# Kernel optimization log

Hardware: AMD Instinct MI355X
Metric: run time of the kernel (lower is better)

## Reference

```python
import jax, jax.numpy as jnp
import numpy as np

N, IN_DIM, HEADS, OUT_DIM = 100000, 128, 4, 32
E = 1600000
NEG_SLOPE = 0.2

def setup_inputs() -> dict:
    key = jax.random.key(0)
    k1, k2, k3, k4, k5 = jax.random.split(key, 5)
    x = jax.random.normal(k1, (N, IN_DIM), dtype=jnp.float32)
    edge_index = jax.random.randint(k2, (2, E), 0, N, dtype=jnp.int32)
    # xavier-like init for params
    W = jax.random.uniform(k3, (IN_DIM, HEADS * OUT_DIM), dtype=jnp.float32,
                           minval=-1.0, maxval=1.0) * np.sqrt(6.0 / (IN_DIM + HEADS * OUT_DIM))
    a_src = jax.random.uniform(k4, (HEADS, OUT_DIM), dtype=jnp.float32,
                               minval=-1.0, maxval=1.0) * np.sqrt(6.0 / (HEADS + OUT_DIM))
    a_dst = jax.random.uniform(k5, (HEADS, OUT_DIM), dtype=jnp.float32,
                               minval=-1.0, maxval=1.0) * np.sqrt(6.0 / (HEADS + OUT_DIM))
    return {"x": x, "edge_index": edge_index, "W": W, "a_src": a_src, "a_dst": a_dst}

def reference(x, edge_index, W, a_src, a_dst):
    src, dst = edge_index[0], edge_index[1]
    n = x.shape[0]
    h = (x @ W).reshape(n, HEADS, OUT_DIM)                      # (N,H,D)
    # per-node attention score halves, then gather per edge (avoids E x D gather twice)
    s_src = jnp.einsum('nhd,hd->nh', h, a_src)                  # (N,H)
    s_dst = jnp.einsum('nhd,hd->nh', h, a_dst)                  # (N,H)
    e = s_src[src] + s_dst[dst]                                 # (E,H)
    e = jnp.where(e > 0, e, NEG_SLOPE * e)                      # leaky_relu(0.2)
    # segment softmax over edges sharing the same dst, per head
    max_per_dst = jax.ops.segment_max(e, dst, num_segments=n)   # (N,H)
    exp = jnp.exp(e - max_per_dst[dst])                         # (E,H)
    denom = jax.ops.segment_sum(exp, dst, num_segments=n)       # (N,H)
    alpha = exp / (denom[dst] + 1e-9)                           # (E,H)
    msg = h[src] * alpha[:, :, None]                            # (E,H,D)
    out = jax.ops.segment_sum(msg, dst, num_segments=n)         # (N,H,D)
    return out.reshape(n, HEADS * OUT_DIM)                      # concat=True
```

## Files before the change

kernel.cpp:

```cpp
#include <hip/hip_runtime.h>
#include <hip/hip_bf16.h>
#include <stdint.h>

#define N_NODES 100000
#define NE 1600000
#define NEG_SLOPE 0.2f
#define NSTRIP 6250
#define NGROUP 49
#define GCAP 34816
#define NFB 64
#define NBKT 3136
#define CAP 768
#define NCTR (NGROUP * 32 + NBKT)

typedef __attribute__((ext_vector_type(8))) short bf16x8;
typedef __attribute__((ext_vector_type(4))) float f32x4;
typedef __attribute__((ext_vector_type(2))) float f32x2;
typedef __attribute__((ext_vector_type(4))) uint32_t u32x4;
typedef __attribute__((ext_vector_type(2))) uint32_t u32x2;

__device__ __forceinline__ short f2bf(float f) {
    __hip_bfloat16 b = __float2bfloat16(f);
    short s; __builtin_memcpy(&s, &b, 2); return s;
}

__global__ __launch_bounds__(256) void k_prep(const float* __restrict__ W,
                                              const float* __restrict__ a_src,
                                              const float* __restrict__ a_dst,
                                              float* __restrict__ vv,
                                              short* __restrict__ wbf,
                                              int* __restrict__ ctrs) {
    const int t = threadIdx.x;
    if (blockIdx.x == 0) {
        if (t < 128) {
            const float* wrow = W + t * 128;
            #pragma unroll
            for (int hd = 0; hd < 4; ++hd) {
                float va = 0.f, vd = 0.f;
                #pragma unroll
                for (int d = 0; d < 32; ++d) {
                    float w = wrow[hd * 32 + d];
                    va += w * a_src[hd * 32 + d];
                    vd += w * a_dst[hd * 32 + d];
                }
                vv[t * 8 + hd]     = va;
                vv[t * 8 + 4 + hd] = vd;
            }
        }
        #pragma unroll 4
        for (int i = 0; i < 64; ++i) {
            int idx = t + i * 256;
            int k = idx >> 7, c = idx & 127;
            int byte = ((c << 8) + (k << 1)) ^ ((c & 7) << 4);
            *(short*)((char*)wbf + byte) = f2bf(W[idx]);
        }
    } else {
        for (int i = t; i < NCTR; i += 256) ctrs[i] = 0;
    }
}

__global__ __launch_bounds__(256) void k_gemm(const float* __restrict__ x,
                                              const short* __restrict__ wbf,
                                              const float* __restrict__ vv,
                                              unsigned char* __restrict__ h8,
                                              float* __restrict__ scales,
                                              float* __restrict__ sv) {
    __shared__ short wt[16384];
    __shared__ float vvl[1024];
    __shared__ float sc[64];
    const int t = threadIdx.x;

    {
        const int4* wsrc = (const int4*)wbf;
        int4* wdst = (int4*)wt;
        #pragma unroll
        for (int i = 0; i < 8; ++i) wdst[t + i * 256] = wsrc[t + i * 256];
    }
    *(f32x4*)(vvl + t * 4) = *(const f32x4*)(vv + t * 4);
    __syncthreads();

    const int wid = t >> 6, lane = t & 63;
    const int strip = blockIdx.x * 4 + wid;
    const bool active = strip < NSTRIP;
    const int r0 = strip * 16;
    const int lr = lane & 15, lg = lane >> 4;

    f32x4 acc[8];
    #pragma unroll
    for (int ct = 0; ct < 8; ++ct) acc[ct] = (f32x4){0.f, 0.f, 0.f, 0.f};
    float part[8];
    #pragma unroll
    for (int i = 0; i < 8; ++i) part[i] = 0.f;

    if (active) {
        bf16x8 a[4];
        #pragma unroll
        for (int kk = 0; kk < 4; ++kk) {
            const float* xp = x + (size_t)(r0 + lr) * 128 + kk * 32 + lg * 8;
            f32x4 x0 = *(const f32x4*)xp;
            f32x4 x1 = *(const f32x4*)(xp + 4);
            int kbase = kk * 32 + lg * 8;
            #pragma unroll
            for (int j = 0; j < 4; ++j) {
                a[kk][j]     = f2bf(x0[j]);
                a[kk][4 + j] = f2bf(x1[j]);
                f32x4 v0 = *(const f32x4*)(vvl + (kbase + j) * 8);
                f32x4 v1 = *(const f32x4*)(vvl + (kbase + j) * 8 + 4);
                f32x4 w0 = *(const f32x4*)(vvl + (kbase + 4 + j) * 8);
                f32x4 w1 = *(const f32x4*)(vvl + (kbase + 4 + j) * 8 + 4);
                #pragma unroll
                for (int i = 0; i < 4; ++i) {
                    part[i]     += x0[j] * v0[i] + x1[j] * w0[i];
                    part[4 + i] += x0[j] * v1[i] + x1[j] * w1[i];
                }
            }
        }
        #pragma unroll
        for (int ct = 0; ct < 8; ++ct) {
            int c = ct * 16 + lr;
            #pragma unroll
            for (int kk = 0; kk < 4; ++kk) {
                int byte = ((c << 8) + ((kk * 32 + lg * 8) << 1)) ^ ((c & 7) << 4);
                bf16x8 b = *(const bf16x8*)((char*)wt + byte);
                acc[ct] = __builtin_amdgcn_mfma_f32_16x16x32_bf16(a[kk], b, acc[ct], 0, 0, 0);
            }
        }
    }
    #pragma unroll
    for (int i = 0; i < 8; ++i) {
        part[i] += __shfl_xor(part[i], 16);
        part[i] += __shfl_xor(part[i], 32);
    }
    if (active && lg == 0) {
        f32x4 s0, s1;
        #pragma unroll
        for (int j = 0; j < 4; ++j) { s0[j] = part[j]; s1[j] = part[4 + j]; }
        *(f32x4*)(sv + (size_t)(r0 + lr) * 8)     = s0;
        *(f32x4*)(sv + (size_t)(r0 + lr) * 8 + 4) = s1;
    }
    if (active) {
        #pragma unroll
        for (int j = 0; j < 4; ++j) {
            float rm = 0.f;
            #pragma unroll
            for (int ct = 0; ct < 8; ++ct) rm = fmaxf(rm, fabsf(acc[ct][j]));
            #pragma unroll
            for (int off2 = 1; off2 < 16; off2 <<= 1)
                rm = fmaxf(rm, __shfl_xor(rm, off2));
            if (lr == 0) {
                scales[r0 + lg * 4 + j] = rm * (1.f / 127.f);
                sc[wid * 16 + lg * 4 + j] = 127.f / fmaxf(rm, 1e-20f);
            }
        }
    }
    __syncthreads();
    if (active) {
        #pragma unroll
        for (int ct = 0; ct < 8; ++ct) {
            #pragma unroll
            for (int j = 0; j < 4; ++j) {
                int row = wid * 16 + lg * 4 + j;
                wt[row * 128 + ct * 16 + lr] = f2bf(acc[ct][j]);
            }
        }
    }
    __syncthreads();
    const int R0 = blockIdx.x * 64;
    #pragma unroll
    for (int it = 0; it < 2; ++it) {
        int sidx = (it * 256 + t) * 16;
        int lrow = sidx >> 7, ch0 = sidx & 127;
        int grow = R0 + lrow;
        if (grow < N_NODES) {
            float invs = sc[lrow];
            u32x4 dws;
            #pragma unroll
            for (int d = 0; d < 4; ++d) {
                uint32_t dw = 0;
                #pragma unroll
                for (int bb = 0; bb < 4; ++bb) {
                    union { uint32_t i; float f; } uu;
                    uu.i = ((uint32_t)(uint16_t)wt[sidx + d * 4 + bb]) << 16;
                    float q = rintf(uu.f * invs);
                    q = fminf(fmaxf(q, -127.f), 127.f);
                    dw |= ((uint32_t)(int)(q + 128.f)) << (8 * bb);
                }
                dws[d] = dw;
            }
            *(u32x4*)(h8 + (size_t)grow * 128 + ch0) = dws;
        }
    }
}

__global__ __launch_bounds__(256) void k_part1(const int* __restrict__ ei,
                                               int* __restrict__ gcur,
                                               int* __restrict__ arena) {
    __shared__ int hist[NGROUP];
    __shared__ int lstart[NGROUP + 1];
    __shared__ int gb[NGROUP];
    __shared__ int binned[4096];
    const int t = threadIdx.x;
    const int e4b = blockIdx.x * 1024;
    if (t < NGROUP) hist[t] = 0;
    __syncthreads();
    int pk[16], gr[16], pl[16];
    #pragma unroll
    for (int i = 0; i < 4; ++i) {
        int e4 = e4b + i * 256 + t;
        bool v = e4 < NE / 4;
        int4 s4 = {0, 0, 0, 0}, d4 = {0, 0, 0, 0};
        if (v) {
            s4 = *(const int4*)(ei + (size_t)e4 * 4);
            d4 = *(const int4*)(ei + NE + (size_t)e4 * 4);
        }
#define P1(k, sf, df) { \
        if (v) { int g = (df) >> 11; gr[i*4+k] = g; \
                 pk[i*4+k] = ((sf) << 11) | ((df) & 2047); \
                 pl[i*4+k] = atomicAdd(&hist[g], 1); } else gr[i*4+k] = -1; }
        P1(0, s4.x, d4.x) P1(1, s4.y, d4.y) P1(2, s4.z, d4.z) P1(3, s4.w, d4.w)
#undef P1
    }
    __syncthreads();
    if (t < 64) {
        int v = (t < NGROUP) ? hist[t] : 0;
        int incl = v;
        #pragma unroll
        for (int off = 1; off < 64; off <<= 1) {
            int y = __shfl_up(incl, off);
            if (t >= off) incl += y;
        }
        if (t < NGROUP) lstart[t + 1] = incl;
        if (t == 0) lstart[0] = 0;
    }
    __syncthreads();
    if (t < NGROUP) gb[t] = atomicAdd(&gcur[t * 32], hist[t]);
    #pragma unroll
    for (int j = 0; j < 16; ++j)
        if (gr[j] >= 0) binned[lstart[gr[j]] + pl[j]] = pk[j];
    __syncthreads();
    const int lane = t & 63, wid = t >> 6;
    for (int g = wid; g < NGROUP; g += 4) {
        int base = gb[g];
        int n = min(hist[g], GCAP - base);
        const int ls = lstart[g];
        int* dst = arena + (size_t)g * GCAP + base;
        for (int i = lane; i < n; i += 64) dst[i] = binned[ls + i];
    }
}

__global__ __launch_bounds__(256) void k_part2(const int* __restrict__ gcur,
                                               const int* __restrict__ arena,
                                               int* __restrict__ bcur,
                                               int* __restrict__ tmp2) {
    const int g = blockIdx.x / 9, chunk = blockIdx.x - g * 9;
    const int cnt = min(gcur[g * 32], GCAP);
    const int cb = chunk * 4096;
    if (cb >= cnt) return;
    __shared__ int hist[NFB];
    __shared__ int lstart[NFB + 1];
    __shared__ int gb[NFB];
    __shared__ int binned[4096];
    const int t = threadIdx.x;
    if (t < NFB) hist[t] = 0;
    __syncthreads();
    int pk[16], fb[16], pl[16];
    const int* ga = arena + (size_t)g * GCAP;
    #pragma unroll
    for (int i = 0; i < 4; ++i) {
        int i4 = cb / 4 + i * 256 + t;
        bool v4 = (i4 * 4) < cnt;
        int4 w4 = {0, 0, 0, 0};
        if (v4) w4 = *(const int4*)(ga + (size_t)i4 * 4);
#define P2(k, wf) { int idx = i4 * 4 + k; \
        if (v4 && idx < cnt) { int f = ((wf) & 2047) >> 5; fb[i*4+k] = f; \
            pk[i*4+k] = (((wf) >> 11) << 5) | ((wf) & 31); \
            pl[i*4+k] = atomicAdd(&hist[f], 1); } else fb[i*4+k] = -1; }
        P2(0, w4.x) P2(1, w4.y) P2(2, w4.z) P2(3, w4.w)
#undef P2
    }
    __syncthreads();
    if (t < 64) {
        int v = hist[t];
        int incl = v;
        #pragma unroll
        for (int off = 1; off < 64; off <<= 1) {
            int y = __shfl_up(incl, off);
            if (t >= off) incl += y;
        }
        lstart[t + 1] = incl;
        if (t == 0) lstart[0] = 0;
    }
    __syncthreads();
    if (t < NFB) gb[t] = atomicAdd(&bcur[g * 64 + t], hist[t]);
    #pragma unroll
    for (int j = 0; j < 16; ++j)
        if (fb[j] >= 0) binned[lstart[fb[j]] + pl[j]] = pk[j];
    __syncthreads();
    const int lane = t & 63, wid = t >> 6;
    for (int f = wid; f < NFB; f += 4) {
        int base = gb[f];
        int n = min(hist[f], CAP - base);
        const int ls = lstart[f];
        int* dst = tmp2 + (size_t)(g * 64 + f) * CAP + base;
        for (int i = lane; i < n; i += 64) dst[i] = binned[ls + i];
    }
}

__global__ __launch_bounds__(256) void k_aggregate(const unsigned char* __restrict__ h8,
                                                   const float* __restrict__ scales,
                                                   const float* __restrict__ sv,
                                                   const int* __restrict__ bcur,
                                                   const int* __restrict__ tmp2,
                                                   float* __restrict__ out) {
    const int b = blockIdx.x;
    const int base = (b >> 6) * 2048 + (b & 63) * 32;
    if (base >= N_NODES) return;
    __shared__ int sorted[CAP];
    __shared__ float wbuf[CAP * 4];
    __shared__ float sbuf[CAP];
    __shared__ int cstart[33];
    __shared__ int ccnt[32];
    __shared__ f32x4 svd4[32];
    const int t = threadIdx.x;
    if (t < 32) {
        ccnt[t] = 0;
        svd4[t] = *(const f32x4*)(sv + (size_t)(base + t) * 8 + 4);
    }
    __syncthreads();
    const int cnt = min(bcur[b], CAP);
    const int* mytmp = tmp2 + (size_t)b * CAP;
    int e0 = -1, e1 = -1, e2 = -1, q0 = 0, q1 = 0, q2 = 0;
    if (t < cnt)       { e0 = mytmp[t];       q0 = atomicAdd(&ccnt[e0 & 31], 1); }
    if (t + 256 < cnt) { e1 = mytmp[t + 256]; q1 = atomicAdd(&ccnt[e1 & 31], 1); }
    if (t + 512 < cnt) { e2 = mytmp[t + 512]; q2 = atomicAdd(&ccnt[e2 & 31], 1); }
    __syncthreads();
    if (t < 64) {
        int v = (t < 32) ? ccnt[t] : 0;
        int incl = v;
        #pragma unroll
        for (int off = 1; off < 32; off <<= 1) {
            int y = __shfl_up(incl, off);
            if (t >= off) incl += y;
        }
        if (t < 32) cstart[t + 1] = incl;
        if (t == 0) cstart[0] = 0;
    }
    __syncthreads();
#define PLACE(e, q) { \
        int pos = cstart[(e) & 31] + (q); \
        sorted[pos] = (e); \
        sbuf[pos] = scales[(size_t)((e) >> 5)]; \
        f32x4 ss = *(const f32x4*)(sv + (size_t)((e) >> 5) * 8); \
        f32x4 sd = svd4[(e) & 31]; \
        f32x4 w4; \
        _Pragma("unroll") \
        for (int hh2 = 0; hh2 < 4; ++hh2) { \
            float v = ss[hh2] + sd[hh2]; \
            v = v > 0.f ? v : NEG_SLOPE * v; \
            w4[hh2] = __expf(v); \
        } \
        *(f32x4*)(wbuf + pos * 4) = w4; }
    if (e0 >= 0) PLACE(e0, q0)
    if (e1 >= 0) PLACE(e1, q1)
    if (e2 >= 0) PLACE(e2, q2)
#undef PLACE
    __syncthreads();

    const int lane = t & 63, wid = t >> 6;
    const int sg = lane >> 4, sl = lane & 15;
    const int hh = sl >> 2;
    const int sgid = wid * 4 + sg;
    const u32x2* hp2 = (const u32x2*)h8;
    #pragma unroll
    for (int rr = 0; rr < 2; ++rr) {
        const int r = sgid * 2 + rr;
        const int s0 = cstart[r], s1 = cstart[r + 1];
        f32x2 a01 = {0.f, 0.f}, a23 = {0.f, 0.f};
        f32x2 a45 = {0.f, 0.f}, a67 = {0.f, 0.f};
        float wsum = 0.f, aws = 0.f;
        for (int j = s0; j < s1; j += 4) {
            int j1 = j + 1 < s1 ? j + 1 : j;
            int j2 = j + 2 < s1 ? j + 2 : j;
            int j3 = j + 3 < s1 ? j + 3 : j;
            int eA = sorted[j], eB = sorted[j1], eC = sorted[j2], eD = sorted[j3];
            u32x2 p0 = hp2[(size_t)(eA >> 5) * 16 + sl];
            u32x2 p1 = hp2[(size_t)(eB >> 5) * 16 + sl];
            u32x2 p2 = hp2[(size_t)(eC >> 5) * 16 + sl];
            u32x2 p3 = hp2[(size_t)(eD >> 5) * 16 + sl];
            float w0 = wbuf[j * 4 + hh];
            float w1 = j + 1 < s1 ? wbuf[j1 * 4 + hh] : 0.f;
            float w2 = j + 2 < s1 ? wbuf[j2 * 4 + hh] : 0.f;
            float w3 = j + 3 < s1 ? wbuf[j3 * 4 + hh] : 0.f;
            float ws0 = w0 * sbuf[j];
            float ws1 = w1 * sbuf[j1];
            float ws2 = w2 * sbuf[j2];
            float ws3 = w3 * sbuf[j3];
#define ACCI(p, ws) { \
            f32x2 ww = {(ws), (ws)}; \
            a01 += ww * (f32x2){(float)((p)[0] & 255u), (float)(((p)[0] >> 8) & 255u)}; \
            a23 += ww * (f32x2){(float)(((p)[0] >> 16) & 255u), (float)((p)[0] >> 24)}; \
            a45 += ww * (f32x2){(float)((p)[1] & 255u), (float)(((p)[1] >> 8) & 255u)}; \
            a67 += ww * (f32x2){(float)(((p)[1] >> 16) & 255u), (float)((p)[1] >> 24)}; }
            ACCI(p0, ws0) ACCI(p1, ws1) ACCI(p2, ws2) ACCI(p3, ws3)
#undef ACCI
            wsum += w0 + w1 + w2 + w3;
            aws  += ws0 + ws1 + ws2 + ws3;
        }
        float inv = 1.f / (wsum + 1e-9f);
        float corr = 128.f * aws;
        float* op = out + (size_t)(base + r) * 128 + sl * 8;
        *(f32x4*)op       = (f32x4){(a01[0] - corr) * inv, (a01[1] - corr) * inv,
                                    (a23[0] - corr) * inv, (a23[1] - corr) * inv};
        *(f32x4*)(op + 4) = (f32x4){(a45[0] - corr) * inv, (a45[1] - corr) * inv,
                                    (a67[0] - corr) * inv, (a67[1] - corr) * inv};
    }
}

extern "C" void kernel_launch(void* const* d_in, const int* in_sizes, int n_in,
                              void* d_out, int out_size, void* d_ws, size_t ws_size,
                              hipStream_t stream) {
    const float* x     = (const float*)d_in[0];
    const int*   ei    = (const int*)d_in[1];
    const float* W     = (const float*)d_in[2];
    const float* a_src = (const float*)d_in[3];
    const float* a_dst = (const float*)d_in[4];
    float* out = (float*)d_out;

    char* ws = (char*)d_ws;
    size_t off = 0;
    auto alloc = [&](size_t bytes) {
        char* p = ws + off;
        off += (bytes + 255) & ~(size_t)255;
        return p;
    };
    unsigned char* h8 = (unsigned char*)alloc((size_t)N_NODES * 128);
    float* scales     = (float*)alloc((size_t)N_NODES * 4);
    float* sv         = (float*)alloc((size_t)N_NODES * 8 * 4);
    float* vv         = (float*)alloc(1024 * 4);
    short* wbf        = (short*)alloc(16384 * 2);
    int* ctrs         = (int*)alloc((size_t)NCTR * 4);
    int* tmp2         = (int*)alloc((size_t)NBKT * CAP * 4);
    int* gcur         = ctrs;
    int* bcur         = ctrs + NGROUP * 32;
    int* arena        = (int*)d_out;

    k_prep<<<2, 256, 0, stream>>>(W, a_src, a_dst, vv, wbf, ctrs);
    k_gemm<<<(NSTRIP + 3) / 4, 256, 0, stream>>>(x, wbf, vv, h8, scales, sv);
    k_part1<<<(NE + 4095) / 4096, 256, 0, stream>>>(ei, gcur, arena);
    k_part2<<<NGROUP * 9, 256, 0, stream>>>(gcur, arena, bcur, tmp2);
    k_aggregate<<<NBKT, 256, 0, stream>>>(h8, scales, sv, bcur, tmp2, out);
}
```

Baseline: 131.0 us.

## Fold attention score projections into MFMA GEMM and unroll aggregate gather by eight

```diff
diff --git a/kernel.cpp b/kernel.cpp
--- a/kernel.cpp
+++ b/kernel.cpp
@@ -24,14 +24,23 @@
     short s; __builtin_memcpy(&s, &b, 2); return s;
 }
 
+__device__ __forceinline__ int wimg_byte(int c, int k) {
+    return ((c << 8) + (k << 1)) ^ ((c & 7) << 4);
+}
+
 __global__ __launch_bounds__(256) void k_prep(const float* __restrict__ W,
                                               const float* __restrict__ a_src,
                                               const float* __restrict__ a_dst,
-                                              float* __restrict__ vv,
                                               short* __restrict__ wbf,
                                               int* __restrict__ ctrs) {
     const int t = threadIdx.x;
     if (blockIdx.x == 0) {
+        #pragma unroll 4
+        for (int i = 0; i < 64; ++i) {
+            int idx = t + i * 256;
+            int k = idx >> 7, c = idx & 127;
+            *(short*)((char*)wbf + wimg_byte(c, k)) = f2bf(W[idx]);
+        }
         if (t < 128) {
             const float* wrow = W + t * 128;
             #pragma unroll
@@ -43,16 +52,12 @@
                     va += w * a_src[hd * 32 + d];
                     vd += w * a_dst[hd * 32 + d];
                 }
-                vv[t * 8 + hd]     = va;
-                vv[t * 8 + 4 + hd] = vd;
-            }
-        }
-        #pragma unroll 4
-        for (int i = 0; i < 64; ++i) {
-            int idx = t + i * 256;
-            int k = idx >> 7, c = idx & 127;
-            int byte = ((c << 8) + (k << 1)) ^ ((c & 7) << 4);
-            *(short*)((char*)wbf + byte) = f2bf(W[idx]);
+                *(short*)((char*)wbf + wimg_byte(128 + hd, t)) = f2bf(va);
+                *(short*)((char*)wbf + wimg_byte(132 + hd, t)) = f2bf(vd);
+            }
+            #pragma unroll
+            for (int c = 136; c < 144; ++c)
+                *(short*)((char*)wbf + wimg_byte(c, t)) = 0;
         }
     } else {
         for (int i = t; i < NCTR; i += 256) ctrs[i] = 0;
@@ -61,12 +66,10 @@
 
 __global__ __launch_bounds__(256) void k_gemm(const float* __restrict__ x,
                                               const short* __restrict__ wbf,
-                                              const float* __restrict__ vv,
                                               unsigned char* __restrict__ h8,
                                               float* __restrict__ scales,
                                               float* __restrict__ sv) {
-    __shared__ short wt[16384];
-    __shared__ float vvl[1024];
+    __shared__ short wt[18432];
     __shared__ float sc[64];
     const int t = threadIdx.x;
 
@@ -74,9 +77,8 @@
         const int4* wsrc = (const int4*)wbf;
         int4* wdst = (int4*)wt;
         #pragma unroll
-        for (int i = 0; i < 8; ++i) wdst[t + i * 256] = wsrc[t + i * 256];
-    }
-    *(f32x4*)(vvl + t * 4) = *(const f32x4*)(vv + t * 4);
+        for (int i = 0; i < 9; ++i) wdst[t + i * 256] = wsrc[t + i * 256];
+    }
     __syncthreads();
 
     const int wid = t >> 6, lane = t & 63;
@@ -85,12 +87,9 @@
     const int r0 = strip * 16;
     const int lr = lane & 15, lg = lane >> 4;
 
-    f32x4 acc[8];
-    #pragma unroll
-    for (int ct = 0; ct < 8; ++ct) acc[ct] = (f32x4){0.f, 0.f, 0.f, 0.f};
-    float part[8];
-    #pragma unroll
-    for (int i = 0; i < 8; ++i) part[i] = 0.f;
+    f32x4 acc[9];
+    #pragma unroll
+    for (int ct = 0; ct < 9; ++ct) acc[ct] = (f32x4){0.f, 0.f, 0.f, 0.f};
 
     if (active) {
         bf16x8 a[4];
@@ -99,44 +98,26 @@
             const float* xp = x + (size_t)(r0 + lr) * 128 + kk * 32 + lg * 8;
             f32x4 x0 = *(const f32x4*)xp;
             f32x4 x1 = *(const f32x4*)(xp + 4);
-            int kbase = kk * 32 + lg * 8;
             #pragma unroll
             for (int j = 0; j < 4; ++j) {
                 a[kk][j]     = f2bf(x0[j]);
                 a[kk][4 + j] = f2bf(x1[j]);
-                f32x4 v0 = *(const f32x4*)(vvl + (kbase + j) * 8);
-                f32x4 v1 = *(const f32x4*)(vvl + (kbase + j) * 8 + 4);
-                f32x4 w0 = *(const f32x4*)(vvl + (kbase + 4 + j) * 8);
-                f32x4 w1 = *(const f32x4*)(vvl + (kbase + 4 + j) * 8 + 4);
-                #pragma unroll
-                for (int i = 0; i < 4; ++i) {
-                    part[i]     += x0[j] * v0[i] + x1[j] * w0[i];
-                    part[4 + i] += x0[j] * v1[i] + x1[j] * w1[i];
-                }
-            }
-        }
-        #pragma unroll
-        for (int ct = 0; ct < 8; ++ct) {
+            }
+        }
+        #pragma unroll
+        for (int ct = 0; ct < 9; ++ct) {
             int c = ct * 16 + lr;
             #pragma unroll
             for (int kk = 0; kk < 4; ++kk) {
-                int byte = ((c << 8) + ((kk * 32 + lg * 8) << 1)) ^ ((c & 7) << 4);
-                bf16x8 b = *(const bf16x8*)((char*)wt + byte);
+                bf16x8 b = *(const bf16x8*)((char*)wt + wimg_byte(c, kk * 32 + lg * 8));
                 acc[ct] = __builtin_amdgcn_mfma_f32_16x16x32_bf16(a[kk], b, acc[ct], 0, 0, 0);
             }
         }
     }
-    #pragma unroll
-    for (int i = 0; i < 8; ++i) {
-        part[i] += __shfl_xor(part[i], 16);
-        part[i] += __shfl_xor(part[i], 32);
-    }
-    if (active && lg == 0) {
-        f32x4 s0, s1;
-        #pragma unroll
-        for (int j = 0; j < 4; ++j) { s0[j] = part[j]; s1[j] = part[4 + j]; }
-        *(f32x4*)(sv + (size_t)(r0 + lr) * 8)     = s0;
-        *(f32x4*)(sv + (size_t)(r0 + lr) * 8 + 4) = s1;
+    if (active && lr < 8) {
+        #pragma unroll
+        for (int j = 0; j < 4; ++j)
+            sv[(size_t)(r0 + lg * 4 + j) * 8 + lr] = acc[8][j];
     }
     if (active) {
         #pragma unroll
@@ -378,33 +359,30 @@
         f32x2 a01 = {0.f, 0.f}, a23 = {0.f, 0.f};
         f32x2 a45 = {0.f, 0.f}, a67 = {0.f, 0.f};
         float wsum = 0.f, aws = 0.f;
-        for (int j = s0; j < s1; j += 4) {
-            int j1 = j + 1 < s1 ? j + 1 : j;
-            int j2 = j + 2 < s1 ? j + 2 : j;
-            int j3 = j + 3 < s1 ? j + 3 : j;
-            int eA = sorted[j], eB = sorted[j1], eC = sorted[j2], eD = sorted[j3];
-            u32x2 p0 = hp2[(size_t)(eA >> 5) * 16 + sl];
-            u32x2 p1 = hp2[(size_t)(eB >> 5) * 16 + sl];
-            u32x2 p2 = hp2[(size_t)(eC >> 5) * 16 + sl];
-            u32x2 p3 = hp2[(size_t)(eD >> 5) * 16 + sl];
-            float w0 = wbuf[j * 4 + hh];
-            float w1 = j + 1 < s1 ? wbuf[j1 * 4 + hh] : 0.f;
-            float w2 = j + 2 < s1 ? wbuf[j2 * 4 + hh] : 0.f;
-            float w3 = j + 3 < s1 ? wbuf[j3 * 4 + hh] : 0.f;
-            float ws0 = w0 * sbuf[j];
-            float ws1 = w1 * sbuf[j1];
-            float ws2 = w2 * sbuf[j2];
-            float ws3 = w3 * sbuf[j3];
-#define ACCI(p, ws) { \
-            f32x2 ww = {(ws), (ws)}; \
-            a01 += ww * (f32x2){(float)((p)[0] & 255u), (float)(((p)[0] >> 8) & 255u)}; \
-            a23 += ww * (f32x2){(float)(((p)[0] >> 16) & 255u), (float)((p)[0] >> 24)}; \
-            a45 += ww * (f32x2){(float)((p)[1] & 255u), (float)(((p)[1] >> 8) & 255u)}; \
-            a67 += ww * (f32x2){(float)(((p)[1] >> 16) & 255u), (float)((p)[1] >> 24)}; }
-            ACCI(p0, ws0) ACCI(p1, ws1) ACCI(p2, ws2) ACCI(p3, ws3)
-#undef ACCI
-            wsum += w0 + w1 + w2 + w3;
-            aws  += ws0 + ws1 + ws2 + ws3;
+        for (int j = s0; j < s1; j += 8) {
+            int jj[8]; int e[8]; u32x2 p[8];
+            #pragma unroll
+            for (int u = 0; u < 8; ++u) jj[u] = (j + u < s1) ? j + u : s1 - 1;
+            #pragma unroll
+            for (int u = 0; u < 8; ++u) e[u] = sorted[jj[u]];
+            #pragma unroll
+            for (int u = 0; u < 8; ++u) p[u] = hp2[(size_t)(e[u] >> 5) * 16 + sl];
+            float w[8], ws[8];
+            #pragma unroll
+            for (int u = 0; u < 8; ++u) {
+                w[u] = (j + u < s1) ? wbuf[jj[u] * 4 + hh] : 0.f;
+                ws[u] = w[u] * sbuf[jj[u]];
+            }
+            #pragma unroll
+            for (int u = 0; u < 8; ++u) {
+                f32x2 ww = {ws[u], ws[u]};
+                a01 += ww * (f32x2){(float)(p[u][0] & 255u), (float)((p[u][0] >> 8) & 255u)};
+                a23 += ww * (f32x2){(float)((p[u][0] >> 16) & 255u), (float)(p[u][0] >> 24)};
+                a45 += ww * (f32x2){(float)(p[u][1] & 255u), (float)((p[u][1] >> 8) & 255u)};
+                a67 += ww * (f32x2){(float)((p[u][1] >> 16) & 255u), (float)(p[u][1] >> 24)};
+                wsum += w[u];
+                aws  += ws[u];
+            }
         }
         float inv = 1.f / (wsum + 1e-9f);
         float corr = 128.f * aws;
@@ -436,16 +414,15 @@
     unsigned char* h8 = (unsigned char*)alloc((size_t)N_NODES * 128);
     float* scales     = (float*)alloc((size_t)N_NODES * 4);
     float* sv         = (float*)alloc((size_t)N_NODES * 8 * 4);
-    float* vv         = (float*)alloc(1024 * 4);
-    short* wbf        = (short*)alloc(16384 * 2);
+    short* wbf        = (short*)alloc(18432 * 2);
     int* ctrs         = (int*)alloc((size_t)NCTR * 4);
     int* tmp2         = (int*)alloc((size_t)NBKT * CAP * 4);
     int* gcur         = ctrs;
     int* bcur         = ctrs + NGROUP * 32;
     int* arena        = (int*)d_out;
 
-    k_prep<<<2, 256, 0, stream>>>(W, a_src, a_dst, vv, wbf, ctrs);
-    k_gemm<<<(NSTRIP + 3) / 4, 256, 0, stream>>>(x, wbf, vv, h8, scales, sv);
+    k_prep<<<2, 256, 0, stream>>>(W, a_src, a_dst, wbf, ctrs);
+    k_gemm<<<(NSTRIP + 3) / 4, 256, 0, stream>>>(x, wbf, h8, scales, sv);
     k_part1<<<(NE + 4095) / 4096, 256, 0, stream>>>(ei, gcur, arena);
     k_part2<<<NGROUP * 9, 256, 0, stream>>>(gcur, arena, bcur, tmp2);
     k_aggregate<<<NBKT, 256, 0, stream>>>(h8, scales, sv, bcur, tmp2, out);
```

Result: faster. 112.1 us (-14.4%).
